# Performance work log

Measured on AMD Instinct MI355X. Metric: run time of the kernel, lower is better.

Reference implementation:

```python
import jax, jax.numpy as jnp
import numpy as np

EPS = 1e-06
H, D_MODEL = 16, 1024
DK = D_MODEL // H
B, S = 16, 4096


def elu_fea_map(x):
    return jax.nn.elu(x) + 1.0


def setup_inputs() -> dict:
    key = jax.random.key(0)
    ks = jax.random.split(key, 11)
    lim = 1.0 / np.sqrt(D_MODEL)
    u = lambda k, shp: jax.random.uniform(k, shp, jnp.float32, -lim, lim)
    return {
        "query": jax.random.normal(ks[0], (B, D_MODEL), jnp.float32),
        "key": jax.random.normal(ks[1], (B, S, D_MODEL), jnp.float32),
        "value": jax.random.normal(ks[2], (B, S, D_MODEL), jnp.float32),
        "Wq": u(ks[3], (D_MODEL, D_MODEL)), "bq": u(ks[4], (D_MODEL,)),
        "Wk": u(ks[5], (D_MODEL, D_MODEL)), "bk": u(ks[6], (D_MODEL,)),
        "Wv": u(ks[7], (D_MODEL, D_MODEL)), "bv": u(ks[8], (D_MODEL,)),
        "Wo": u(ks[9], (D_MODEL, D_MODEL)), "bo": u(ks[10], (D_MODEL,)),
    }


def reference(query, key, value, Wq, bq, Wk, bk, Wv, bv, Wo, bo):
    nb = query.shape[0]
    # projections; torch Linear: x @ W.T + b
    q = (query @ Wq.T + bq).reshape(nb, 1, H, DK)   # [B,1,H,D]
    k = (key @ Wk.T + bk).reshape(nb, -1, H, DK)    # [B,S,H,D]
    v = (value @ Wv.T + bv).reshape(nb, -1, H, DK)  # [B,S,H,M]
    Q = elu_fea_map(q)
    K = elu_fea_map(k)
    KV = jnp.einsum('bshd,bshm->bhdm', K, v)                      # [B,H,D,M]
    Z = 1.0 / (jnp.einsum('bshd,bhd->bsh', Q, K.sum(axis=1)) + EPS)  # [B,1,H]
    V = jnp.einsum('bshd,bhdm,bsh->bshm', Q, KV, Z)               # [B,1,H,M]
    x = V.reshape(nb, H * DK)
    return x @ Wo.T + bo
```

## Files before the change

kernel.cpp:

```cpp
#include <hip/hip_runtime.h>
#include <hip/hip_bf16.h>
#include <stdint.h>


using bf16 = __hip_bfloat16;
typedef __attribute__((ext_vector_type(8))) short short8;
typedef __attribute__((ext_vector_type(4))) float f32x4;

#define NB_B 16
#define SEQ 4096
#define DM 1024
#define NH 16
#define DKH 64

__device__ __forceinline__ void gload_lds16(const void* g, void* l) {
  __builtin_amdgcn_global_load_lds((const __attribute__((address_space(1))) void*)g,
                                   (__attribute__((address_space(3))) void*)l, 16, 0, 0);
}

__global__ __launch_bounds__(256) void conv_kernel(const float* __restrict__ src,
                                                   bf16* __restrict__ dst, long n4) {
  long i = (long)blockIdx.x * blockDim.x + threadIdx.x;
  const long stride = (long)gridDim.x * blockDim.x;
  for (; i < n4; i += stride) {
    float4 v = ((const float4*)src)[i];
    union { ushort4 u; bf16 h[4]; } o;
    o.h[0] = __float2bfloat16(v.x);
    o.h[1] = __float2bfloat16(v.y);
    o.h[2] = __float2bfloat16(v.z);
    o.h[3] = __float2bfloat16(v.w);
    ((ushort4*)dst)[i] = o.u;
  }
}

template <int KPROJ>
__global__ __launch_bounds__(512, 1) void gemm256(
    const bf16* __restrict__ A, const bf16* __restrict__ W,
    const float* __restrict__ bias, bf16* __restrict__ outT,
    float* __restrict__ Ksum, int rowsTot, int b0, int chunk) {
  __shared__ bf16 As[2][256 * 64];
  __shared__ bf16 Bs[2][256 * 64];
  const int tid = threadIdx.x;
  const int lane = tid & 63;
  const int wid = tid >> 6;
  const int wr = wid >> 2;
  const int wc = wid & 3;
  const int wgid = (blockIdx.x & 7) * chunk + (blockIdx.x >> 3);
  const int row0 = (wgid >> 2) * 256;
  const int col0 = (wgid & 3) * 256;

  f32x4 acc[8][4] = {};

  const int bsrc = ((lane & 7) ^ (lane >> 3)) * 8;
  const int xr = (lane & 7) << 4;
  const int lr = lane & 15;
  const int lk = (lane >> 4) * 16;

  const bf16* Ab = A + (long)(row0 + wid * 32 + (lane >> 3)) * DM + bsrc;
  const bf16* Wb = W + (long)(col0 + wid * 32 + (lane >> 3)) * DM + bsrc;
  const int sdst = (wid * 32) * 64;

#pragma unroll
  for (int j = 0; j < 4; ++j)
    gload_lds16(Ab + (long)j * 8 * DM, (void*)&As[0][sdst + j * 512]);
#pragma unroll
  for (int j = 0; j < 4; ++j)
    gload_lds16(Wb + (long)j * 8 * DM, (void*)&Bs[0][sdst + j * 512]);
  asm volatile("s_waitcnt vmcnt(0)\n\ts_barrier" ::: "memory");

  short8 af[4], bfv[4];

  for (int kt = 0; kt < 16; ++kt) {
    const int cur = kt & 1;
    const char* Asc = (const char*)As[cur];
    const char* Bsc = (const char*)Bs[cur];
    bf16* Asn = As[cur ^ 1];
    bf16* Bsn = Bs[cur ^ 1];
    const long kbn = (kt + 1) * 64;

    if (kt < 15) {
#pragma unroll
      for (int j = 0; j < 4; ++j)
        gload_lds16(Ab + (long)j * 8 * DM + kbn, (void*)&Asn[sdst + j * 512]);
      asm volatile("s_waitcnt vmcnt(4)\n\ts_barrier" ::: "memory");
    } else {
      asm volatile("s_waitcnt vmcnt(0)\n\ts_barrier" ::: "memory");
    }
#pragma unroll
    for (int m = 0; m < 4; ++m)
      af[m] = *(const short8*)(Asc + (wr * 128 + m * 16 + lr) * 128 + (lk ^ xr));
#pragma unroll
    for (int n = 0; n < 4; ++n)
      bfv[n] = *(const short8*)(Bsc + (wc * 64 + n * 16 + lr) * 128 + (lk ^ xr));
    __builtin_amdgcn_sched_barrier(0);
    __builtin_amdgcn_s_setprio(1);
#pragma unroll
    for (int m = 0; m < 4; ++m)
#pragma unroll
      for (int n = 0; n < 4; ++n)
        acc[m][n] = __builtin_amdgcn_mfma_f32_16x16x32_bf16(af[m], bfv[n], acc[m][n], 0, 0, 0);
    __builtin_amdgcn_s_setprio(0);
    asm volatile("s_barrier" ::: "memory");

#pragma unroll
    for (int m = 0; m < 4; ++m)
      af[m] = *(const short8*)(Asc + (wr * 128 + (m + 4) * 16 + lr) * 128 + (lk ^ xr));
    if (kt < 15) {
#pragma unroll
      for (int j = 0; j < 4; ++j)
        gload_lds16(Wb + (long)j * 8 * DM + kbn, (void*)&Bsn[sdst + j * 512]);
    }
    asm volatile("s_barrier" ::: "memory");
    __builtin_amdgcn_sched_barrier(0);
    __builtin_amdgcn_s_setprio(1);
#pragma unroll
    for (int m = 0; m < 4; ++m)
#pragma unroll
      for (int n = 0; n < 4; ++n)
        acc[m + 4][n] = __builtin_amdgcn_mfma_f32_16x16x32_bf16(af[m], bfv[n], acc[m + 4][n], 0, 0, 0);
    __builtin_amdgcn_s_setprio(0);
    asm volatile("s_barrier" ::: "memory");

#pragma unroll
    for (int m = 0; m < 4; ++m)
      af[m] = *(const short8*)(Asc + (wr * 128 + m * 16 + lr) * 128 + ((64 + lk) ^ xr));
#pragma unroll
    for (int n = 0; n < 4; ++n)
      bfv[n] = *(const short8*)(Bsc + (wc * 64 + n * 16 + lr) * 128 + ((64 + lk) ^ xr));
    asm volatile("s_barrier" ::: "memory");
    __builtin_amdgcn_sched_barrier(0);
    __builtin_amdgcn_s_setprio(1);
#pragma unroll
    for (int m = 0; m < 4; ++m)
#pragma unroll
      for (int n = 0; n < 4; ++n)
        acc[m][n] = __builtin_amdgcn_mfma_f32_16x16x32_bf16(af[m], bfv[n], acc[m][n], 0, 0, 0);
    __builtin_amdgcn_s_setprio(0);
    asm volatile("s_barrier" ::: "memory");

#pragma unroll
    for (int m = 0; m < 4; ++m)
      af[m] = *(const short8*)(Asc + (wr * 128 + (m + 4) * 16 + lr) * 128 + ((64 + lk) ^ xr));
    asm volatile("s_barrier" ::: "memory");
    __builtin_amdgcn_sched_barrier(0);
    __builtin_amdgcn_s_setprio(1);
#pragma unroll
    for (int m = 0; m < 4; ++m)
#pragma unroll
      for (int n = 0; n < 4; ++n)
        acc[m + 4][n] = __builtin_amdgcn_mfma_f32_16x16x32_bf16(af[m], bfv[n], acc[m + 4][n], 0, 0, 0);
    __builtin_amdgcn_s_setprio(0);
    asm volatile("s_barrier" ::: "memory");
  }

  const int bglob = b0 + (row0 >> 12);
#pragma unroll
  for (int n = 0; n < 4; ++n) {
    const int colg = col0 + wc * 64 + n * 16 + lr;
    const float bv = bias[colg];
    float csum = 0.f;
#pragma unroll
    for (int m = 0; m < 8; ++m) {
      const int r = row0 + wr * 128 + m * 16 + (lane >> 4) * 4;
      union { ushort4 u; bf16 h[4]; } pk;
#pragma unroll
      for (int i = 0; i < 4; ++i) {
        float v = acc[m][n][i] + bv;
        if (KPROJ) { v = v > 0.f ? v + 1.f : __expf(v); csum += v; }
        pk.h[i] = __float2bfloat16(v);
      }
      *(ushort4*)&outT[(long)colg * rowsTot + r] = pk.u;
    }
    if (KPROJ) {
      csum += __shfl_xor(csum, 16);
      csum += __shfl_xor(csum, 32);
      if (lane < 16) atomicAdd(&Ksum[(long)bglob * DM + colg], csum);
    }
  }
}

__global__ __launch_bounds__(256) void kv_kernel(
    const bf16* __restrict__ KT, const bf16* __restrict__ VT,
    float* __restrict__ KVp, int rowsTot, int b0) {
  const int sp = blockIdx.x & 3;
  const int h = (blockIdx.x >> 2) & 15;
  const int b_loc = blockIdx.x >> 6;
  const int lane = threadIdx.x & 63;
  const int w = threadIdx.x >> 6;
  const long srow = (long)b_loc * SEQ + sp * (SEQ / 4) + ((lane >> 4) * 8);
  const bf16* Ab = KT + (long)(h * DKH + w * 16 + (lane & 15)) * rowsTot + srow;
  const bf16* Bb = VT + (long)(h * DKH + (lane & 15)) * rowsTot + srow;
  f32x4 acc[4] = {};
#pragma unroll 2
  for (int s = 0; s < SEQ / 4; s += 32) {
    short8 a = *(const short8*)(Ab + s);
#pragma unroll
    for (int n = 0; n < 4; ++n) {
      short8 bv = *(const short8*)(Bb + (long)n * 16 * rowsTot + s);
      acc[n] = __builtin_amdgcn_mfma_f32_16x16x32_bf16(a, bv, acc[n], 0, 0, 0);
    }
  }
  float* o = KVp + (((long)sp * NB_B + (b0 + b_loc)) * NH + h) * DKH * DKH;
#pragma unroll
  for (int n = 0; n < 4; ++n)
#pragma unroll
    for (int i = 0; i < 4; ++i)
      o[(w * 16 + (lane >> 4) * 4 + i) * DKH + n * 16 + (lane & 15)] = acc[n][i];
}

template <int ELU>
__global__ __launch_bounds__(256) void vecmat_kernel(
    const float* __restrict__ in, const float* __restrict__ W,
    const float* __restrict__ bias, float* __restrict__ outp) {
  const int b = blockIdx.x >> 5;
  const int n0 = (blockIdx.x & 31) * 32;
  const int lane = threadIdx.x & 63;
  const int w = threadIdx.x >> 6;
  float4 qv[4];
#pragma unroll
  for (int it = 0; it < 4; ++it)
    qv[it] = *(const float4*)&in[(long)b * DM + it * 256 + lane * 4];
#pragma unroll
  for (int j = 0; j < 8; ++j) {
    const int n = n0 + w * 8 + j;
    const float* wrow = W + (long)n * DM;
    float s = 0.f;
#pragma unroll
    for (int it = 0; it < 4; ++it) {
      float4 wv = *(const float4*)&wrow[it * 256 + lane * 4];
      s += qv[it].x * wv.x + qv[it].y * wv.y + qv[it].z * wv.z + qv[it].w * wv.w;
    }
    s += __shfl_xor(s, 1);  s += __shfl_xor(s, 2);  s += __shfl_xor(s, 4);
    s += __shfl_xor(s, 8);  s += __shfl_xor(s, 16); s += __shfl_xor(s, 32);
    if (lane == 0) {
      float v = s + bias[n];
      if (ELU) v = v > 0.f ? v + 1.f : __expf(v);
      outp[(long)b * DM + n] = v;
    }
  }
}

__global__ __launch_bounds__(256) void xcomp_kernel(
    const float* __restrict__ Q, const float* __restrict__ KVp,
    const float* __restrict__ Ksum, float* __restrict__ xb) {
  const int b = blockIdx.x;
  const int t = threadIdx.x;
  const int h = t >> 4;
  const int m0 = (t & 15) * 4;
  const float* q = Q + (long)b * DM + h * DKH;
  const float* ks = Ksum + (long)b * DM + h * DKH;
  const long kvoff = ((long)b * NH + h) * DKH * DKH;
  const long spstride = (long)NB_B * NH * DKH * DKH;
  float zden = 0.f;
#pragma unroll
  for (int d = 0; d < DKH; ++d) zden += q[d] * ks[d];
  const float z = 1.f / (zden + 1e-6f);
  float nv[4] = {0.f, 0.f, 0.f, 0.f};
  for (int d = 0; d < DKH; ++d) {
    const float qd = q[d];
#pragma unroll
    for (int j = 0; j < 4; ++j) {
      const long idx = kvoff + d * DKH + m0 + j;
      nv[j] += qd * (KVp[idx] + KVp[idx + spstride] +
                     KVp[idx + 2 * spstride] + KVp[idx + 3 * spstride]);
    }
  }
  float* xo = xb + (long)b * DM + h * DKH + m0;
#pragma unroll
  for (int j = 0; j < 4; ++j) xo[j] = nv[j] * z;
}

extern "C" void kernel_launch(void* const* d_in, const int* in_sizes, int n_in,
                              void* d_out, int out_size, void* d_ws, size_t ws_size,
                              hipStream_t stream) {
  (void)in_sizes; (void)n_in; (void)out_size;
  const float* query = (const float*)d_in[0];
  const float* key   = (const float*)d_in[1];
  const float* value = (const float*)d_in[2];
  const float* Wq = (const float*)d_in[3];
  const float* bq = (const float*)d_in[4];
  const float* Wk = (const float*)d_in[5];
  const float* bk = (const float*)d_in[6];
  const float* Wv = (const float*)d_in[7];
  const float* bv = (const float*)d_in[8];
  const float* Wo = (const float*)d_in[9];
  const float* bo = (const float*)d_in[10];
  float* out = (float*)d_out;

  char* p = (char*)d_ws;
  bf16* WkB = (bf16*)p;  p += (size_t)DM * DM * 2;
  bf16* WvB = (bf16*)p;  p += (size_t)DM * DM * 2;
  float* KVp = (float*)p; p += (size_t)4 * NB_B * NH * DKH * DKH * 4;
  float* Ksum = (float*)p; p += (size_t)NB_B * DM * 4;
  float* Q = (float*)p;  p += (size_t)NB_B * DM * 4;
  float* xb = (float*)p; p += (size_t)NB_B * DM * 4;
  const size_t fixed = (size_t)(p - (char*)d_ws);
  const size_t per_b = (size_t)4 * SEQ * DM * 2;
  if (ws_size < fixed + per_b) return;
  int nbc = (int)((ws_size - fixed) / per_b);
  if (nbc > NB_B) nbc = NB_B;
  bf16* keyB = (bf16*)p; p += (size_t)nbc * SEQ * DM * 2;
  bf16* valB = (bf16*)p; p += (size_t)nbc * SEQ * DM * 2;
  bf16* kT   = (bf16*)p; p += (size_t)nbc * SEQ * DM * 2;
  bf16* vT   = (bf16*)p; p += (size_t)nbc * SEQ * DM * 2;

  hipMemsetAsync(Ksum, 0, (size_t)NB_B * DM * 4, stream);
  conv_kernel<<<512, 256, 0, stream>>>(Wk, WkB, (long)DM * DM / 4);
  conv_kernel<<<512, 256, 0, stream>>>(Wv, WvB, (long)DM * DM / 4);
  vecmat_kernel<1><<<NB_B * 32, 256, 0, stream>>>(query, Wq, bq, Q);

  for (int b0 = 0; b0 < NB_B; b0 += nbc) {
    const int nb = (NB_B - b0 < nbc) ? (NB_B - b0) : nbc;
    const int rows = nb * SEQ;
    const long n4 = (long)rows * DM / 4;
    conv_kernel<<<2048, 256, 0, stream>>>(key + (size_t)b0 * SEQ * DM, keyB, n4);
    conv_kernel<<<2048, 256, 0, stream>>>(value + (size_t)b0 * SEQ * DM, valB, n4);
    const int nwg = (rows / 256) * 4;
    gemm256<1><<<nwg, 512, 0, stream>>>(keyB, WkB, bk, kT, Ksum, rows, b0, nwg / 8);
    gemm256<0><<<nwg, 512, 0, stream>>>(valB, WvB, bv, vT, (float*)nullptr, rows, b0, nwg / 8);
    kv_kernel<<<nb * NH * 4, 256, 0, stream>>>(kT, vT, KVp, rows, b0);
  }

  xcomp_kernel<<<NB_B, 256, 0, stream>>>(Q, KVp, Ksum, xb);
  vecmat_kernel<0><<<NB_B * 32, 256, 0, stream>>>(xb, Wo, bo, out);
}
```

Before: 683.8 us.

## Fuse fp32-to-bf16 activation conversion into projection GEMM A-tile loads

Removes the separate conversion passes over key and value. The GEMM now reads fp32 activations straight into registers through a 4-deep prefetch ring, converts them to bf16 and writes them into swizzled LDS. The weight tiles move to a triple-buffered direct-to-LDS pipeline issued two steps ahead, with hand-tuned vmcnt waits. This cuts a full read and write of the bf16 key/value copies and halves the workspace per batch, which may allow larger batch chunks. The cost is doubled global read bytes inside the GEMM, much higher register pressure from the ring, and fragile waitcnt accounting.

```diff
diff --git a/kernel.cpp b/kernel.cpp
--- a/kernel.cpp
+++ b/kernel.cpp
@@ -16,6 +16,15 @@
 __device__ __forceinline__ void gload_lds16(const void* g, void* l) {
   __builtin_amdgcn_global_load_lds((const __attribute__((address_space(1))) void*)g,
                                    (__attribute__((address_space(3))) void*)l, 16, 0, 0);
+}
+
+__device__ __forceinline__ short8 pack_bf16x8(float4 a, float4 b) {
+  union { bf16 h[8]; short8 v; } pk;
+  pk.h[0] = __float2bfloat16(a.x); pk.h[1] = __float2bfloat16(a.y);
+  pk.h[2] = __float2bfloat16(a.z); pk.h[3] = __float2bfloat16(a.w);
+  pk.h[4] = __float2bfloat16(b.x); pk.h[5] = __float2bfloat16(b.y);
+  pk.h[6] = __float2bfloat16(b.z); pk.h[7] = __float2bfloat16(b.w);
+  return pk.v;
 }
 
 __global__ __launch_bounds__(256) void conv_kernel(const float* __restrict__ src,
@@ -35,11 +44,11 @@
 
 template <int KPROJ>
 __global__ __launch_bounds__(512, 1) void gemm256(
-    const bf16* __restrict__ A, const bf16* __restrict__ W,
+    const float* __restrict__ A, const bf16* __restrict__ W,
     const float* __restrict__ bias, bf16* __restrict__ outT,
     float* __restrict__ Ksum, int rowsTot, int b0, int chunk) {
   __shared__ bf16 As[2][256 * 64];
-  __shared__ bf16 Bs[2][256 * 64];
+  __shared__ bf16 Bs[3][256 * 64];
   const int tid = threadIdx.x;
   const int lane = tid & 63;
   const int wid = tid >> 6;
@@ -56,36 +65,51 @@
   const int lr = lane & 15;
   const int lk = (lane >> 4) * 16;
 
-  const bf16* Ab = A + (long)(row0 + wid * 32 + (lane >> 3)) * DM + bsrc;
+  const float* Afp = A + (long)(row0 + wid * 32 + (lane >> 3)) * DM + (lane & 7) * 8;
+  const int awbase = (wid * 32 + (lane >> 3)) * 128 + (((lane & 7) ^ (lane >> 3)) << 4);
   const bf16* Wb = W + (long)(col0 + wid * 32 + (lane >> 3)) * DM + bsrc;
-  const int sdst = (wid * 32) * 64;
-
-#pragma unroll
-  for (int j = 0; j < 4; ++j)
-    gload_lds16(Ab + (long)j * 8 * DM, (void*)&As[0][sdst + j * 512]);
-#pragma unroll
-  for (int j = 0; j < 4; ++j)
-    gload_lds16(Wb + (long)j * 8 * DM, (void*)&Bs[0][sdst + j * 512]);
-  asm volatile("s_waitcnt vmcnt(0)\n\ts_barrier" ::: "memory");
+  const int sdst = wid * 32 * 64;
+
+  float4 ring[4][8];
+
+#define ISSUE_A(slot, kt_) \
+  _Pragma("unroll") for (int j = 0; j < 4; ++j) { \
+    ring[slot][2 * j]     = *(const float4*)(Afp + (long)j * 8 * DM + (kt_) * 64); \
+    ring[slot][2 * j + 1] = *(const float4*)(Afp + (long)j * 8 * DM + (kt_) * 64 + 4); \
+  }
+#define ISSUE_B(buf, kt_) \
+  _Pragma("unroll") for (int j = 0; j < 4; ++j) \
+    gload_lds16(Wb + (long)j * 8 * DM + (kt_) * 64, (void*)&Bs[buf][sdst + j * 512]);
+#define WRITE_A(abuf, slot) \
+  _Pragma("unroll") for (int j = 0; j < 4; ++j) \
+    *(short8*)((char*)As[abuf] + awbase + j * 1024) = \
+        pack_bf16x8(ring[slot][2 * j], ring[slot][2 * j + 1]);
+
+  ISSUE_A(0, 0)
+  ISSUE_A(1, 1)
+  ISSUE_B(0, 0)
+  ISSUE_A(2, 2)
+  ISSUE_B(1, 1)
+  ISSUE_A(3, 3)
+  asm volatile("s_waitcnt vmcnt(32)" ::: "memory");
+  WRITE_A(0, 0)
 
   short8 af[4], bfv[4];
 
+#pragma unroll
   for (int kt = 0; kt < 16; ++kt) {
-    const int cur = kt & 1;
-    const char* Asc = (const char*)As[cur];
-    const char* Bsc = (const char*)Bs[cur];
-    bf16* Asn = As[cur ^ 1];
-    bf16* Bsn = Bs[cur ^ 1];
-    const long kbn = (kt + 1) * 64;
-
-    if (kt < 15) {
-#pragma unroll
-      for (int j = 0; j < 4; ++j)
-        gload_lds16(Ab + (long)j * 8 * DM + kbn, (void*)&Asn[sdst + j * 512]);
-      asm volatile("s_waitcnt vmcnt(4)\n\ts_barrier" ::: "memory");
-    } else {
-      asm volatile("s_waitcnt vmcnt(0)\n\ts_barrier" ::: "memory");
-    }
+    const char* Asc = (const char*)As[kt & 1];
+    const char* Bsc = (const char*)Bs[kt % 3];
+
+    if (kt + 2 < 16) { ISSUE_B((kt + 2) % 3, kt + 2) }
+    if (kt + 4 < 16) { ISSUE_A((kt + 4) & 3, kt + 4) }
+    if (kt <= 12)      asm volatile("s_waitcnt vmcnt(32) lgkmcnt(0)" ::: "memory");
+    else if (kt == 13) asm volatile("s_waitcnt vmcnt(16) lgkmcnt(0)" ::: "memory");
+    else if (kt == 14) asm volatile("s_waitcnt vmcnt(4) lgkmcnt(0)" ::: "memory");
+    else               asm volatile("s_waitcnt vmcnt(0) lgkmcnt(0)" ::: "memory");
+    if (kt + 1 < 16) { WRITE_A((kt + 1) & 1, (kt + 1) & 3) }
+    asm volatile("s_barrier" ::: "memory");
+
 #pragma unroll
     for (int m = 0; m < 4; ++m)
       af[m] = *(const short8*)(Asc + (wr * 128 + m * 16 + lr) * 128 + (lk ^ xr));
@@ -105,11 +129,6 @@
 #pragma unroll
     for (int m = 0; m < 4; ++m)
       af[m] = *(const short8*)(Asc + (wr * 128 + (m + 4) * 16 + lr) * 128 + (lk ^ xr));
-    if (kt < 15) {
-#pragma unroll
-      for (int j = 0; j < 4; ++j)
-        gload_lds16(Wb + (long)j * 8 * DM + kbn, (void*)&Bsn[sdst + j * 512]);
-    }
     asm volatile("s_barrier" ::: "memory");
     __builtin_amdgcn_sched_barrier(0);
     __builtin_amdgcn_s_setprio(1);
@@ -152,6 +171,9 @@
     __builtin_amdgcn_s_setprio(0);
     asm volatile("s_barrier" ::: "memory");
   }
+#undef ISSUE_A
+#undef ISSUE_B
+#undef WRITE_A
 
   const int bglob = b0 + (row0 >> 12);
 #pragma unroll
@@ -295,14 +317,12 @@
   float* Q = (float*)p;  p += (size_t)NB_B * DM * 4;
   float* xb = (float*)p; p += (size_t)NB_B * DM * 4;
   const size_t fixed = (size_t)(p - (char*)d_ws);
-  const size_t per_b = (size_t)4 * SEQ * DM * 2;
+  const size_t per_b = (size_t)2 * SEQ * DM * 2;
   if (ws_size < fixed + per_b) return;
   int nbc = (int)((ws_size - fixed) / per_b);
   if (nbc > NB_B) nbc = NB_B;
-  bf16* keyB = (bf16*)p; p += (size_t)nbc * SEQ * DM * 2;
-  bf16* valB = (bf16*)p; p += (size_t)nbc * SEQ * DM * 2;
-  bf16* kT   = (bf16*)p; p += (size_t)nbc * SEQ * DM * 2;
-  bf16* vT   = (bf16*)p; p += (size_t)nbc * SEQ * DM * 2;
+  bf16* kT = (bf16*)p; p += (size_t)nbc * SEQ * DM * 2;
+  bf16* vT = (bf16*)p; p += (size_t)nbc * SEQ * DM * 2;
 
   hipMemsetAsync(Ksum, 0, (size_t)NB_B * DM * 4, stream);
   conv_kernel<<<512, 256, 0, stream>>>(Wk, WkB, (long)DM * DM / 4);
@@ -312,12 +332,9 @@
   for (int b0 = 0; b0 < NB_B; b0 += nbc) {
     const int nb = (NB_B - b0 < nbc) ? (NB_B - b0) : nbc;
     const int rows = nb * SEQ;
-    const long n4 = (long)rows * DM / 4;
-    conv_kernel<<<2048, 256, 0, stream>>>(key + (size_t)b0 * SEQ * DM, keyB, n4);
-    conv_kernel<<<2048, 256, 0, stream>>>(value + (size_t)b0 * SEQ * DM, valB, n4);
     const int nwg = (rows / 256) * 4;
-    gemm256<1><<<nwg, 512, 0, stream>>>(keyB, WkB, bk, kT, Ksum, rows, b0, nwg / 8);
-    gemm256<0><<<nwg, 512, 0, stream>>>(valB, WvB, bv, vT, (float*)nullptr, rows, b0, nwg / 8);
+    gemm256<1><<<nwg, 512, 0, stream>>>(key + (size_t)b0 * SEQ * DM, WkB, bk, kT, Ksum, rows, b0, nwg / 8);
+    gemm256<0><<<nwg, 512, 0, stream>>>(value + (size_t)b0 * SEQ * DM, WvB, bv, vT, (float*)nullptr, rows, b0, nwg / 8);
     kv_kernel<<<nb * NH * 4, 256, 0, stream>>>(kT, vT, KVp, rows, b0);
   }
 
```

After: 1.302 ms. +90.4%, slower.
